# Performance work log

Measured on AMD Instinct MI355X. Metric: run time of the kernel, lower is better.

The kernel has to match this reference:

```python
import jax, jax.numpy as jnp
import numpy as np

ALPHA = 0.2  # LeakyReLU negative slope
NEG_INF = -9e15  # mask value used by the torch dense GAT layer

def _gat_layer(x, adj, W, a1, a2):
    # x: [N, F], W: [F, Fh], a1/a2: [Fh]
    Wh = x @ W                                   # [N, Fh]
    f1 = Wh @ a1                                 # [N] source scores
    f2 = Wh @ a2                                 # [N] dest scores
    e = jax.nn.leaky_relu(f1[:, None] + f2[None, :], ALPHA)  # [N, N]
    att = jnp.where(adj > 0, e, NEG_INF)
    att = jax.nn.softmax(att, axis=1)
    return att @ Wh                              # [N, Fh]

def setup_inputs():
    key = jax.random.key(0)
    ks = jax.random.split(key, 8)
    N, F, H, Fh, C = 6144, 512, 4, 64, 40
    x = jax.random.normal(ks[0], (N, F), jnp.float32)
    # sparse-ish binary adjacency with self loops (dense storage as in the module)
    adj = (jax.random.uniform(ks[1], (N, N)) < 0.005).astype(jnp.float32)
    adj = jnp.maximum(adj, jnp.eye(N, dtype=jnp.float32))
    s = 1.0 / np.sqrt(Fh)
    W = jax.random.normal(ks[2], (H, F, Fh), jnp.float32) * s
    a1 = jax.random.normal(ks[3], (H, Fh), jnp.float32) * s
    a2 = jax.random.normal(ks[4], (H, Fh), jnp.float32) * s
    so = 1.0 / np.sqrt(C)
    Wo = jax.random.normal(ks[5], (H * Fh, C), jnp.float32) * so
    ao1 = jax.random.normal(ks[6], (C,), jnp.float32) * so
    ao2 = jax.random.normal(ks[7], (C,), jnp.float32) * so
    return {"x": x, "adj": adj, "W": W, "a1": a1, "a2": a2,
            "Wo": Wo, "ao1": ao1, "ao2": ao2}

def reference(x, adj, W, a1, a2, Wo, ao1, ao2):
    N = x.shape[0]
    # multi-head layer (concat=True -> ELU applied inside each head)
    heads = jax.vmap(_gat_layer, in_axes=(None, None, 0, 0, 0))(x, adj, W, a1, a2)  # [H, N, Fh]
    h = jax.nn.elu(heads)
    h = jnp.transpose(h, (1, 0, 2)).reshape(N, -1)   # concat heads -> [N, H*Fh]
    # output attention layer (concat=False), then outer ELU from GAT.forward
    out = jax.nn.elu(_gat_layer(h, adj, Wo, ao1, ao2))  # [N, C]
    return jax.nn.log_softmax(out, axis=1)
```

## Files before the change

kernel.cpp:

```cpp
#include <hip/hip_runtime.h>
#include <stdint.h>

#define N_NODES 6144
#define F_IN 512
#define NHEAD 4
#define FH 64
#define HF 256
#define NCLS 40
#define CAP 192
#define LRELU_ALPHA 0.2f

typedef __bf16 bf16x8 __attribute__((ext_vector_type(8)));
typedef float floatx4 __attribute__((ext_vector_type(4)));

__device__ __forceinline__ uint16_t f2b(float f){
    union { float f; uint32_t i; } x; x.f = f;
    uint32_t r = x.i + 0x7FFFu + ((x.i >> 16) & 1u);
    return (uint16_t)(r >> 16);
}

__global__ void k_cvt_x(const float* __restrict__ x, uint16_t* __restrict__ xb){
    int idx = (blockIdx.x * 256 + threadIdx.x) * 4;
    float4 v = *reinterpret_cast<const float4*>(x + idx);
    ushort4 o;
    o.x = f2b(v.x); o.y = f2b(v.y); o.z = f2b(v.z); o.w = f2b(v.w);
    *reinterpret_cast<ushort4*>(xb + idx) = o;
}

__global__ void k_transpose_w(const float* __restrict__ W, uint16_t* __restrict__ Wt){
    int idx = blockIdx.x * 256 + threadIdx.x;
    int c = idx >> 9, k = idx & 511;
    Wt[idx] = f2b(W[((c >> 6) << 15) + k * 64 + (c & 63)]);
}

__global__ void k_build_csr(const float* __restrict__ adj, int* __restrict__ cnt,
                            int* __restrict__ idxbuf){
    __shared__ int scnt;
    int i = blockIdx.x, t = threadIdx.x;
    if (t == 0) scnt = 0;
    __syncthreads();
    const float4* row = reinterpret_cast<const float4*>(adj + (size_t)i * N_NODES);
    int* out = idxbuf + (size_t)i * CAP;
    for (int q = t; q < N_NODES / 4; q += 256){
        float4 v = row[q];
        int j0 = q * 4;
        if (v.x != 0.f){ int p = atomicAdd(&scnt, 1); if (p < CAP) out[p] = j0;     }
        if (v.y != 0.f){ int p = atomicAdd(&scnt, 1); if (p < CAP) out[p] = j0 + 1; }
        if (v.z != 0.f){ int p = atomicAdd(&scnt, 1); if (p < CAP) out[p] = j0 + 2; }
        if (v.w != 0.f){ int p = atomicAdd(&scnt, 1); if (p < CAP) out[p] = j0 + 3; }
    }
    __syncthreads();
    if (t == 0) cnt[i] = scnt < CAP ? scnt : CAP;
}

__global__ void k_gemm1(const uint16_t* __restrict__ xb, const uint16_t* __restrict__ Wt,
                        float* __restrict__ Wh1){
    int w = threadIdx.x >> 6, l = threadIdx.x & 63;
    int r0 = blockIdx.x * 32 + (w & 1) * 16;
    int c0 = blockIdx.y * 32 + (w >> 1) * 16;
    int m = l & 15, q = l >> 4;
    const uint16_t* ap = xb + (size_t)(r0 + m) * F_IN + q * 8;
    const uint16_t* bp = Wt + (size_t)(c0 + m) * F_IN + q * 8;
    floatx4 acc = {0.f, 0.f, 0.f, 0.f};
    for (int k0 = 0; k0 < F_IN; k0 += 32){
        bf16x8 a = *reinterpret_cast<const bf16x8*>(ap + k0);
        bf16x8 b = *reinterpret_cast<const bf16x8*>(bp + k0);
        acc = __builtin_amdgcn_mfma_f32_16x16x32_bf16(a, b, acc, 0, 0, 0);
    }
    int col = c0 + m;
    int rowb = r0 + q * 4;
    #pragma unroll
    for (int r = 0; r < 4; r++)
        Wh1[(size_t)(rowb + r) * HF + col] = acc[r];
}

__global__ void k_f12(const float* __restrict__ Wh1, const float* __restrict__ a1,
                      const float* __restrict__ a2, float* __restrict__ f1,
                      float* __restrict__ f2){
    int n = blockIdx.x;
    int h = threadIdx.x >> 6, l = threadIdx.x & 63;
    float w = Wh1[(size_t)n * HF + h * FH + l];
    float s1 = w * a1[h * FH + l];
    float s2 = w * a2[h * FH + l];
    for (int off = 32; off; off >>= 1){
        s1 += __shfl_xor(s1, off);
        s2 += __shfl_xor(s2, off);
    }
    if (l == 0){ f1[h * N_NODES + n] = s1; f2[h * N_NODES + n] = s2; }
}

__global__ void k_attn1(const int* __restrict__ cnt, const int* __restrict__ idxbuf,
                        const float* __restrict__ Wh1, const float* __restrict__ f1,
                        const float* __restrict__ f2, float* __restrict__ hcat){
    int i = blockIdx.x, h = blockIdx.y, l = threadIdx.x;
    int c = cnt[i];
    __shared__ int   sidx[CAP];
    __shared__ float sp[CAP];
    const int* src = idxbuf + (size_t)i * CAP;
    for (int e = l; e < c; e += 64) sidx[e] = src[e];
    __syncthreads();
    float f1i = f1[h * N_NODES + i];
    float mx = -1e30f;
    for (int e = l; e < c; e += 64){
        float s = f1i + f2[h * N_NODES + sidx[e]];
        s = s > 0.f ? s : LRELU_ALPHA * s;
        sp[e] = s;
        mx = fmaxf(mx, s);
    }
    for (int off = 32; off; off >>= 1) mx = fmaxf(mx, __shfl_xor(mx, off));
    __syncthreads();
    float ssum = 0.f;
    for (int e = l; e < c; e += 64){
        float p = __expf(sp[e] - mx);
        sp[e] = p;
        ssum += p;
    }
    for (int off = 32; off; off >>= 1) ssum += __shfl_xor(ssum, off);
    float inv = 1.f / ssum;
    __syncthreads();
    float acc = 0.f;
    const float* whb = Wh1 + h * FH + l;
    for (int e = 0; e < c; e++)
        acc += sp[e] * inv * whb[(size_t)sidx[e] * HF];
    float v = acc > 0.f ? acc : __expf(acc) - 1.f;
    hcat[(size_t)i * HF + h * FH + l] = v;
}

__global__ void k_gemm2(const float* __restrict__ hcat, const float* __restrict__ Wo,
                        const float* __restrict__ ao1, const float* __restrict__ ao2,
                        float* __restrict__ Wh2, float* __restrict__ f1o,
                        float* __restrict__ f2o){
    int w = threadIdx.x >> 6, l = threadIdx.x & 63;
    int n = blockIdx.x * 4 + w;
    const float* hr = hcat + (size_t)n * HF;
    float acc = 0.f;
    if (l < NCLS){
        for (int k = 0; k < HF; k++)
            acc += hr[k] * Wo[k * NCLS + l];
    }
    float t1 = l < NCLS ? acc * ao1[l] : 0.f;
    float t2 = l < NCLS ? acc * ao2[l] : 0.f;
    for (int off = 32; off; off >>= 1){
        t1 += __shfl_xor(t1, off);
        t2 += __shfl_xor(t2, off);
    }
    if (l < NCLS) Wh2[(size_t)n * NCLS + l] = acc;
    if (l == 0){ f1o[n] = t1; f2o[n] = t2; }
}

__global__ void k_attn2(const int* __restrict__ cnt, const int* __restrict__ idxbuf,
                        const float* __restrict__ Wh2, const float* __restrict__ f1o,
                        const float* __restrict__ f2o, float* __restrict__ out){
    int i = blockIdx.x, l = threadIdx.x;
    int c = cnt[i];
    __shared__ int   sidx[CAP];
    __shared__ float sp[CAP];
    const int* src = idxbuf + (size_t)i * CAP;
    for (int e = l; e < c; e += 64) sidx[e] = src[e];
    __syncthreads();
    float f1i = f1o[i];
    float mx = -1e30f;
    for (int e = l; e < c; e += 64){
        float s = f1i + f2o[sidx[e]];
        s = s > 0.f ? s : LRELU_ALPHA * s;
        sp[e] = s;
        mx = fmaxf(mx, s);
    }
    for (int off = 32; off; off >>= 1) mx = fmaxf(mx, __shfl_xor(mx, off));
    __syncthreads();
    float ssum = 0.f;
    for (int e = l; e < c; e += 64){
        float p = __expf(sp[e] - mx);
        sp[e] = p;
        ssum += p;
    }
    for (int off = 32; off; off >>= 1) ssum += __shfl_xor(ssum, off);
    float inv = 1.f / ssum;
    __syncthreads();
    float acc = 0.f;
    if (l < NCLS){
        for (int e = 0; e < c; e++)
            acc += sp[e] * inv * Wh2[(size_t)sidx[e] * NCLS + l];
    }
    float o = (l < NCLS) ? (acc > 0.f ? acc : __expf(acc) - 1.f) : -1e30f;
    float m2 = o;
    for (int off = 32; off; off >>= 1) m2 = fmaxf(m2, __shfl_xor(m2, off));
    float ex = (l < NCLS) ? __expf(o - m2) : 0.f;
    for (int off = 32; off; off >>= 1) ex += __shfl_xor(ex, off);
    float res = o - m2 - logf(ex);
    if (l < NCLS) out[(size_t)i * NCLS + l] = res;
}

extern "C" void kernel_launch(void* const* d_in, const int* in_sizes, int n_in,
                              void* d_out, int out_size, void* d_ws, size_t ws_size,
                              hipStream_t stream) {
    const float* x   = (const float*)d_in[0];
    const float* adj = (const float*)d_in[1];
    const float* W   = (const float*)d_in[2];
    const float* a1  = (const float*)d_in[3];
    const float* a2  = (const float*)d_in[4];
    const float* Wo  = (const float*)d_in[5];
    const float* ao1 = (const float*)d_in[6];
    const float* ao2 = (const float*)d_in[7];
    float* out = (float*)d_out;

    char* ws = (char*)d_ws;
    int*      nbr_cnt = (int*)     (ws + 0);
    int*      nbr_idx = (int*)     (ws + 24576);
    uint16_t* Wt      = (uint16_t*)(ws + 4743168);
    uint16_t* xb      = (uint16_t*)(ws + 5005312);
    float*    Wh1     = (float*)   (ws + 11296768);
    float*    f1      = (float*)   (ws + 17588224);
    float*    f2      = (float*)   (ws + 17686528);
    float*    hcat    = (float*)   (ws + 17784832);
    float*    Wh2     = (float*)   (ws + 24076288);
    float*    f1o     = (float*)   (ws + 25059328);
    float*    f2o     = (float*)   (ws + 25083904);

    hipLaunchKernelGGL(k_cvt_x,       dim3(3072),       dim3(256), 0, stream, x, xb);
    hipLaunchKernelGGL(k_transpose_w, dim3(512),        dim3(256), 0, stream, W, Wt);
    hipLaunchKernelGGL(k_build_csr,   dim3(6144),       dim3(256), 0, stream, adj, nbr_cnt, nbr_idx);
    hipLaunchKernelGGL(k_gemm1,       dim3(192, 8),     dim3(256), 0, stream, xb, Wt, Wh1);
    hipLaunchKernelGGL(k_f12,         dim3(6144),       dim3(256), 0, stream, Wh1, a1, a2, f1, f2);
    hipLaunchKernelGGL(k_attn1,       dim3(6144, 4),    dim3(64),  0, stream, nbr_cnt, nbr_idx, Wh1, f1, f2, hcat);
    hipLaunchKernelGGL(k_gemm2,       dim3(1536),       dim3(256), 0, stream, hcat, Wo, ao1, ao2, Wh2, f1o, f2o);
    hipLaunchKernelGGL(k_attn2,       dim3(6144),       dim3(64),  0, stream, nbr_cnt, nbr_idx, Wh2, f1o, f2o, out);
}
```

Measured before the change: 318.7 us.

## Split bf16 GEMM into hi/lo parts, fuse prep kernels, unroll attention gathers

The input conversion now writes split bf16 hi/lo pairs for x and W, and gemm1 issues three MFMAs per step so the first projection runs at near-fp32 accuracy. The x/W conversion kernels and a new Wo transpose are merged into one prep kernel. Both attention aggregation loops are unrolled by four with independent gathers and the softmax normalisation is moved out of the loop. gemm2 reads a transposed Wo with float4 loads. The precision fix triples MFMA work and doubles the bf16 traffic in gemm1 and prep, which offsets the gains from the other changes.

```diff
diff --git a/kernel.cpp b/kernel.cpp
--- a/kernel.cpp
+++ b/kernel.cpp
@@ -13,24 +13,43 @@
 typedef __bf16 bf16x8 __attribute__((ext_vector_type(8)));
 typedef float floatx4 __attribute__((ext_vector_type(4)));
 
+__device__ __forceinline__ float b2f(uint16_t u){
+    union { float f; uint32_t i; } x; x.i = ((uint32_t)u) << 16; return x.f;
+}
 __device__ __forceinline__ uint16_t f2b(float f){
     union { float f; uint32_t i; } x; x.f = f;
     uint32_t r = x.i + 0x7FFFu + ((x.i >> 16) & 1u);
     return (uint16_t)(r >> 16);
 }
 
-__global__ void k_cvt_x(const float* __restrict__ x, uint16_t* __restrict__ xb){
-    int idx = (blockIdx.x * 256 + threadIdx.x) * 4;
-    float4 v = *reinterpret_cast<const float4*>(x + idx);
-    ushort4 o;
-    o.x = f2b(v.x); o.y = f2b(v.y); o.z = f2b(v.z); o.w = f2b(v.w);
-    *reinterpret_cast<ushort4*>(xb + idx) = o;
-}
-
-__global__ void k_transpose_w(const float* __restrict__ W, uint16_t* __restrict__ Wt){
-    int idx = blockIdx.x * 256 + threadIdx.x;
-    int c = idx >> 9, k = idx & 511;
-    Wt[idx] = f2b(W[((c >> 6) << 15) + k * 64 + (c & 63)]);
+__global__ void k_prep(const float* __restrict__ x, const float* __restrict__ W,
+                       const float* __restrict__ Wo,
+                       uint16_t* __restrict__ xh, uint16_t* __restrict__ xl,
+                       uint16_t* __restrict__ Wth, uint16_t* __restrict__ Wtl,
+                       float* __restrict__ Wot){
+    int b = blockIdx.x, t = threadIdx.x;
+    if (b < 3072){
+        int idx = (b * 256 + t) * 4;
+        float4 v = *reinterpret_cast<const float4*>(x + idx);
+        ushort4 hi, lo;
+        hi.x = f2b(v.x); lo.x = f2b(v.x - b2f(hi.x));
+        hi.y = f2b(v.y); lo.y = f2b(v.y - b2f(hi.y));
+        hi.z = f2b(v.z); lo.z = f2b(v.z - b2f(hi.z));
+        hi.w = f2b(v.w); lo.w = f2b(v.w - b2f(hi.w));
+        *reinterpret_cast<ushort4*>(xh + idx) = hi;
+        *reinterpret_cast<ushort4*>(xl + idx) = lo;
+    } else if (b < 3584){
+        int idx = (b - 3072) * 256 + t;
+        int c = idx >> 9, k = idx & 511;
+        float v = W[((c >> 6) << 15) + k * 64 + (c & 63)];
+        uint16_t hi = f2b(v);
+        Wth[idx] = hi;
+        Wtl[idx] = f2b(v - b2f(hi));
+    } else {
+        int idx = (b - 3584) * 256 + t;
+        int l = idx >> 8, k = idx & 255;
+        Wot[idx] = Wo[k * NCLS + l];
+    }
 }
 
 __global__ void k_build_csr(const float* __restrict__ adj, int* __restrict__ cnt,
@@ -53,19 +72,28 @@
     if (t == 0) cnt[i] = scnt < CAP ? scnt : CAP;
 }
 
-__global__ void k_gemm1(const uint16_t* __restrict__ xb, const uint16_t* __restrict__ Wt,
+__global__ void k_gemm1(const uint16_t* __restrict__ xh, const uint16_t* __restrict__ xl,
+                        const uint16_t* __restrict__ Wth, const uint16_t* __restrict__ Wtl,
                         float* __restrict__ Wh1){
     int w = threadIdx.x >> 6, l = threadIdx.x & 63;
     int r0 = blockIdx.x * 32 + (w & 1) * 16;
     int c0 = blockIdx.y * 32 + (w >> 1) * 16;
     int m = l & 15, q = l >> 4;
-    const uint16_t* ap = xb + (size_t)(r0 + m) * F_IN + q * 8;
-    const uint16_t* bp = Wt + (size_t)(c0 + m) * F_IN + q * 8;
+    size_t aoff = (size_t)(r0 + m) * F_IN + q * 8;
+    size_t boff = (size_t)(c0 + m) * F_IN + q * 8;
+    const uint16_t* ahp = xh  + aoff;
+    const uint16_t* alp = xl  + aoff;
+    const uint16_t* bhp = Wth + boff;
+    const uint16_t* blp = Wtl + boff;
     floatx4 acc = {0.f, 0.f, 0.f, 0.f};
     for (int k0 = 0; k0 < F_IN; k0 += 32){
-        bf16x8 a = *reinterpret_cast<const bf16x8*>(ap + k0);
-        bf16x8 b = *reinterpret_cast<const bf16x8*>(bp + k0);
-        acc = __builtin_amdgcn_mfma_f32_16x16x32_bf16(a, b, acc, 0, 0, 0);
+        bf16x8 ah = *reinterpret_cast<const bf16x8*>(ahp + k0);
+        bf16x8 al = *reinterpret_cast<const bf16x8*>(alp + k0);
+        bf16x8 bh = *reinterpret_cast<const bf16x8*>(bhp + k0);
+        bf16x8 bl = *reinterpret_cast<const bf16x8*>(blp + k0);
+        acc = __builtin_amdgcn_mfma_f32_16x16x32_bf16(ah, bl, acc, 0, 0, 0);
+        acc = __builtin_amdgcn_mfma_f32_16x16x32_bf16(al, bh, acc, 0, 0, 0);
+        acc = __builtin_amdgcn_mfma_f32_16x16x32_bf16(ah, bh, acc, 0, 0, 0);
     }
     int col = c0 + m;
     int rowb = r0 + q * 4;
@@ -120,23 +148,41 @@
     __syncthreads();
     float acc = 0.f;
     const float* whb = Wh1 + h * FH + l;
-    for (int e = 0; e < c; e++)
-        acc += sp[e] * inv * whb[(size_t)sidx[e] * HF];
+    int e = 0;
+    for (; e + 4 <= c; e += 4){
+        int j0 = sidx[e], j1 = sidx[e+1], j2 = sidx[e+2], j3 = sidx[e+3];
+        float v0 = whb[(size_t)j0 * HF];
+        float v1 = whb[(size_t)j1 * HF];
+        float v2 = whb[(size_t)j2 * HF];
+        float v3 = whb[(size_t)j3 * HF];
+        acc += sp[e]*v0 + sp[e+1]*v1 + sp[e+2]*v2 + sp[e+3]*v3;
+    }
+    for (; e < c; e++)
+        acc += sp[e] * whb[(size_t)sidx[e] * HF];
+    acc *= inv;
     float v = acc > 0.f ? acc : __expf(acc) - 1.f;
     hcat[(size_t)i * HF + h * FH + l] = v;
 }
 
-__global__ void k_gemm2(const float* __restrict__ hcat, const float* __restrict__ Wo,
+__global__ void k_gemm2(const float* __restrict__ hcat, const float* __restrict__ Wot,
                         const float* __restrict__ ao1, const float* __restrict__ ao2,
                         float* __restrict__ Wh2, float* __restrict__ f1o,
                         float* __restrict__ f2o){
     int w = threadIdx.x >> 6, l = threadIdx.x & 63;
     int n = blockIdx.x * 4 + w;
-    const float* hr = hcat + (size_t)n * HF;
+    const float4* hr4 = reinterpret_cast<const float4*>(hcat + (size_t)n * HF);
     float acc = 0.f;
     if (l < NCLS){
-        for (int k = 0; k < HF; k++)
-            acc += hr[k] * Wo[k * NCLS + l];
+        const float4* wr4 = reinterpret_cast<const float4*>(Wot + (size_t)l * HF);
+        float a0 = 0.f, a1 = 0.f;
+        #pragma unroll 8
+        for (int k = 0; k < HF / 4; k += 2){
+            float4 h0 = hr4[k],     w0 = wr4[k];
+            float4 h1 = hr4[k + 1], w1 = wr4[k + 1];
+            a0 += h0.x*w0.x + h0.y*w0.y + h0.z*w0.z + h0.w*w0.w;
+            a1 += h1.x*w1.x + h1.y*w1.y + h1.z*w1.z + h1.w*w1.w;
+        }
+        acc = a0 + a1;
     }
     float t1 = l < NCLS ? acc * ao1[l] : 0.f;
     float t2 = l < NCLS ? acc * ao2[l] : 0.f;
@@ -179,8 +225,19 @@
     __syncthreads();
     float acc = 0.f;
     if (l < NCLS){
-        for (int e = 0; e < c; e++)
-            acc += sp[e] * inv * Wh2[(size_t)sidx[e] * NCLS + l];
+        const float* wb = Wh2 + l;
+        int e = 0;
+        for (; e + 4 <= c; e += 4){
+            int j0 = sidx[e], j1 = sidx[e+1], j2 = sidx[e+2], j3 = sidx[e+3];
+            float v0 = wb[(size_t)j0 * NCLS];
+            float v1 = wb[(size_t)j1 * NCLS];
+            float v2 = wb[(size_t)j2 * NCLS];
+            float v3 = wb[(size_t)j3 * NCLS];
+            acc += sp[e]*v0 + sp[e+1]*v1 + sp[e+2]*v2 + sp[e+3]*v3;
+        }
+        for (; e < c; e++)
+            acc += sp[e] * wb[(size_t)sidx[e] * NCLS];
+        acc *= inv;
     }
     float o = (l < NCLS) ? (acc > 0.f ? acc : __expf(acc) - 1.f) : -1e30f;
     float m2 = o;
@@ -207,22 +264,24 @@
     char* ws = (char*)d_ws;
     int*      nbr_cnt = (int*)     (ws + 0);
     int*      nbr_idx = (int*)     (ws + 24576);
-    uint16_t* Wt      = (uint16_t*)(ws + 4743168);
-    uint16_t* xb      = (uint16_t*)(ws + 5005312);
-    float*    Wh1     = (float*)   (ws + 11296768);
-    float*    f1      = (float*)   (ws + 17588224);
-    float*    f2      = (float*)   (ws + 17686528);
-    float*    hcat    = (float*)   (ws + 17784832);
-    float*    Wh2     = (float*)   (ws + 24076288);
-    float*    f1o     = (float*)   (ws + 25059328);
-    float*    f2o     = (float*)   (ws + 25083904);
-
-    hipLaunchKernelGGL(k_cvt_x,       dim3(3072),       dim3(256), 0, stream, x, xb);
-    hipLaunchKernelGGL(k_transpose_w, dim3(512),        dim3(256), 0, stream, W, Wt);
-    hipLaunchKernelGGL(k_build_csr,   dim3(6144),       dim3(256), 0, stream, adj, nbr_cnt, nbr_idx);
-    hipLaunchKernelGGL(k_gemm1,       dim3(192, 8),     dim3(256), 0, stream, xb, Wt, Wh1);
-    hipLaunchKernelGGL(k_f12,         dim3(6144),       dim3(256), 0, stream, Wh1, a1, a2, f1, f2);
-    hipLaunchKernelGGL(k_attn1,       dim3(6144, 4),    dim3(64),  0, stream, nbr_cnt, nbr_idx, Wh1, f1, f2, hcat);
-    hipLaunchKernelGGL(k_gemm2,       dim3(1536),       dim3(256), 0, stream, hcat, Wo, ao1, ao2, Wh2, f1o, f2o);
-    hipLaunchKernelGGL(k_attn2,       dim3(6144),       dim3(64),  0, stream, nbr_cnt, nbr_idx, Wh2, f1o, f2o, out);
-}
+    uint16_t* xh      = (uint16_t*)(ws + 4743168);
+    uint16_t* xl      = (uint16_t*)(ws + 11034624);
+    uint16_t* Wth     = (uint16_t*)(ws + 17326080);
+    uint16_t* Wtl     = (uint16_t*)(ws + 17588224);
+    float*    Wot     = (float*)   (ws + 17850368);
+    float*    Wh1     = (float*)   (ws + 17891328);
+    float*    f1      = (float*)   (ws + 24182784);
+    float*    f2      = (float*)   (ws + 24281088);
+    float*    hcat    = (float*)   (ws + 24379392);
+    float*    Wh2     = (float*)   (ws + 30670848);
+    float*    f1o     = (float*)   (ws + 31653888);
+    float*    f2o     = (float*)   (ws + 31678464);
+
+    hipLaunchKernelGGL(k_prep,      dim3(3624),       dim3(256), 0, stream, x, W, Wo, xh, xl, Wth, Wtl, Wot);
+    hipLaunchKernelGGL(k_build_csr, dim3(6144),       dim3(256), 0, stream, adj, nbr_cnt, nbr_idx);
+    hipLaunchKernelGGL(k_gemm1,     dim3(192, 8),     dim3(256), 0, stream, xh, xl, Wth, Wtl, Wh1);
+    hipLaunchKernelGGL(k_f12,       dim3(6144),       dim3(256), 0, stream, Wh1, a1, a2, f1, f2);
+    hipLaunchKernelGGL(k_attn1,     dim3(6144, 4),    dim3(64),  0, stream, nbr_cnt, nbr_idx, Wh1, f1, f2, hcat);
+    hipLaunchKernelGGL(k_gemm2,     dim3(1536),       dim3(256), 0, stream, hcat, Wot, ao1, ao2, Wh2, f1o, f2o);
+    hipLaunchKernelGGL(k_attn2,     dim3(6144),       dim3(64),  0, stream, nbr_cnt, nbr_idx, Wh2, f1o, f2o, out);
+}
```

After: 352.3 us. 10.5% more time.
